# Optimization experiments

Measured on AMD Instinct MI355X. Metric: run time of the kernel, lower is better.

## Reference

```python
import jax, jax.numpy as jnp
import numpy as np

N, E, D, L = 100000, 600000, 128, 4
BN_EPS = 1e-5


def setup_inputs() -> dict:
    key = jax.random.key(0)
    ks = jax.random.split(key, 16)
    s = 0.02
    inp = {
        "x": jax.random.normal(ks[0], (N, D), dtype=jnp.float32),
        "edge_index": jax.random.randint(ks[1], (2, E), 0, N, dtype=jnp.int64),
        # per-layer SAGEConv params (lin_l has bias, lin_r has no bias in PyG)
        "lin_l_w": jax.random.normal(ks[2], (L, D, D), dtype=jnp.float32) * s,
        "lin_l_b": jnp.zeros((L, D), dtype=jnp.float32),
        "lin_r_w": jax.random.normal(ks[3], (L, D, D), dtype=jnp.float32) * s,
        # BatchNorm affine params (eval mode, running mean=0 var=1)
        "bn_w": jnp.ones((L, D), dtype=jnp.float32),
        "bn_b": jnp.zeros((L, D), dtype=jnp.float32),
        # MLP head: 128 -> 256 -> 128 -> 1
        "fc1_w": jax.random.normal(ks[4], (2 * D, D), dtype=jnp.float32) * s,
        "fc1_b": jnp.zeros((2 * D,), dtype=jnp.float32),
        "fc2_w": jax.random.normal(ks[5], (D, 2 * D), dtype=jnp.float32) * s,
        "fc2_b": jnp.zeros((D,), dtype=jnp.float32),
        "fc3_w": jax.random.normal(ks[6], (1, D), dtype=jnp.float32) * s,
        "fc3_b": jnp.zeros((1,), dtype=jnp.float32),
    }
    return inp


def _sage_layer(h, src, dst, deg_inv, wl, bl, wr):
    # mean aggregation of source features at destination nodes
    agg = jax.ops.segment_sum(h[src], dst, num_segments=N)  # [N, D]
    agg = agg * deg_inv[:, None]
    return agg @ wl.T + bl + h @ wr.T


def reference(x, lin_l_w, lin_l_b, lin_r_w, bn_w, bn_b,
              fc1_w, fc1_b, fc2_w, fc2_b, fc3_w, fc3_b, edge_index):
    src, dst = edge_index[0], edge_index[1]
    deg = jax.ops.segment_sum(jnp.ones((E,), jnp.float32), dst, num_segments=N)
    deg_inv = jnp.where(deg > 0, 1.0 / jnp.maximum(deg, 1.0), 0.0)
    inv_std = 1.0 / jnp.sqrt(1.0 + BN_EPS)  # eval BN with running mean=0, var=1

    h = x
    node_rep = x  # JK='sum' sums h_list[0..L-1]: input + first L-1 layer outputs
    for l in range(L):
        h = _sage_layer(h, src, dst, deg_inv, lin_l_w[l], lin_l_b[l], lin_r_w[l])
        h = h * inv_std * bn_w[l] + bn_b[l]
        if l != L - 1:
            h = jax.nn.relu(h)  # dropout = identity in eval mode
        if l != L - 1:
            node_rep = node_rep + h

    # batch is None -> global_add_pool sums all nodes into one graph
    g = jnp.sum(node_rep, axis=0, keepdims=True)  # [1, D]
    g = jax.nn.relu(g @ fc1_w.T + fc1_b)
    g = jax.nn.relu(g @ fc2_w.T + fc2_b)
    out = g @ fc3_w.T + fc3_b  # [1, num_tasks]
    return out
```

## Files before the change

### kernel.cpp

```cpp
#include <hip/hip_runtime.h>

#define NN 100000
#define NE 600000
#define DD 128
#define SCAN_CHUNK 2048
#define NCHUNK 49

typedef __attribute__((ext_vector_type(8))) short bf8;
typedef __attribute__((ext_vector_type(4))) float f4;
typedef __attribute__((ext_vector_type(4))) unsigned short us4;
typedef __attribute__((ext_vector_type(8))) unsigned short us8;

__device__ __forceinline__ float frelu(float x) { return x > 0.f ? x : 0.f; }

__device__ __forceinline__ float b2f(unsigned short u)
{
    union { unsigned int i; float f; } c;
    c.i = ((unsigned int)u) << 16;
    return c.f;
}

__device__ __forceinline__ unsigned short f2b(float f)
{
    union { float f; unsigned int i; } c;
    c.f = f;
    unsigned int u = c.i;
    return (unsigned short)((u + 0x7fffu + ((u >> 16) & 1u)) >> 16);
}

__device__ __forceinline__ float2 up2(unsigned int v)
{
    return make_float2(__uint_as_float(v << 16),
                       __uint_as_float(v & 0xffff0000u));
}

__global__ void k_detect(const int* __restrict__ ei, int* __restrict__ flag)
{
    if (blockIdx.x == 0 && threadIdx.x == 0) {
        int z = 1;
        for (int i = 0; i < 64; ++i)
            if (ei[2 * i + 1] != 0) { z = 0; break; }
        flag[0] = z;
    }
}

__global__ void k_count(const int* __restrict__ ei, const int* __restrict__ flag,
                        int* __restrict__ deg)
{
    int e = blockIdx.x * 256 + threadIdx.x;
    if (e >= NE) return;
    int w = flag[0];
    int dst = w ? ei[2 * (NE + e)] : ei[NE + e];
    atomicAdd(&deg[dst], 1);
}

__global__ void k_scan1(const int* __restrict__ cnt, int* __restrict__ offs,
                        int* __restrict__ chunks)
{
    __shared__ int sd[256];
    int t = threadIdx.x;
    int base = blockIdx.x * SCAN_CHUNK + t * 8;
    int v[8];
    int s = 0;
    #pragma unroll
    for (int i = 0; i < 8; ++i) {
        int idx = base + i;
        v[i] = (idx < NN) ? cnt[idx] : 0;
        s += v[i];
    }
    sd[t] = s;
    __syncthreads();
    for (int o = 1; o < 256; o <<= 1) {
        int x = (t >= o) ? sd[t - o] : 0;
        __syncthreads();
        sd[t] += x;
        __syncthreads();
    }
    int run = sd[t] - s;
    if (t == 255) chunks[blockIdx.x] = sd[255];
    #pragma unroll
    for (int i = 0; i < 8; ++i) {
        int idx = base + i;
        if (idx < NN) offs[idx] = run;
        run += v[i];
    }
}

__global__ void k_scan2(int* __restrict__ chunks, int* __restrict__ offs)
{
    if (threadIdx.x == 0 && blockIdx.x == 0) {
        int run = 0;
        for (int c = 0; c < NCHUNK; ++c) {
            int v = chunks[c];
            chunks[c] = run;
            run += v;
        }
        offs[NN] = run;
    }
}

__global__ void k_add2(int* __restrict__ offs, const int* __restrict__ chunks,
                       int* __restrict__ cursor, const int* __restrict__ deg,
                       float* __restrict__ deginv)
{
    int i = blockIdx.x * 256 + threadIdx.x;
    if (i >= NN) return;
    int v = offs[i] + chunks[i >> 11];
    offs[i] = v;
    cursor[i] = v;
    int d = deg[i];
    deginv[i] = (d > 0) ? 1.0f / (float)d : 0.0f;
}

__global__ void k_fill(const int* __restrict__ ei, const int* __restrict__ flag,
                       int* __restrict__ cursor, int* __restrict__ csr)
{
    int e = blockIdx.x * 256 + threadIdx.x;
    if (e >= NE) return;
    int w = flag[0];
    int src = w ? ei[2 * e] : ei[e];
    int dst = w ? ei[2 * (NE + e)] : ei[NE + e];
    int p = atomicAdd(&cursor[dst], 1);
    csr[p] = src;
}

__global__ void k_fold(const float* __restrict__ lwl, const float* __restrict__ lbl,
                       const float* __restrict__ lwr, const float* __restrict__ bnw,
                       const float* __restrict__ bnb, unsigned short* __restrict__ w2,
                       float* __restrict__ bias)
{
    int id = blockIdx.x * 256 + threadIdx.x;
    int l = id >> 15;
    int j = (id >> 8) & 127;
    int k = id & 255;
    float inv_std = 1.0f / sqrtf(1.0f + 1e-5f);
    float s = inv_std * bnw[l * 128 + j];
    float w = (k < 128) ? lwl[(l * 128 + j) * 128 + k]
                        : lwr[(l * 128 + j) * 128 + (k - 128)];
    w2[id] = f2b(w * s);
    if (k == 0) bias[l * 128 + j] = lbl[l * 128 + j] * s + bnb[l * 128 + j];
}

__global__ void k_cvtsum(const float* __restrict__ x, unsigned short* __restrict__ xb,
                         float* __restrict__ gsum)
{
    __shared__ float red[16][128];
    const int t = threadIdx.x;
    const int c8 = (t & 15) * 8;
    const int rg = t >> 4;
    float s[8];
    #pragma unroll
    for (int j = 0; j < 8; ++j) s[j] = 0.f;
    for (int r = blockIdx.x * 16 + rg; r < NN; r += gridDim.x * 16) {
        const f4* p = (const f4*)(x + (size_t)r * 128 + c8);
        f4 a = p[0], b = p[1];
        us8 o;
        o[0] = f2b(a[0]); o[1] = f2b(a[1]); o[2] = f2b(a[2]); o[3] = f2b(a[3]);
        o[4] = f2b(b[0]); o[5] = f2b(b[1]); o[6] = f2b(b[2]); o[7] = f2b(b[3]);
        *(us8*)(xb + (size_t)r * 128 + c8) = o;
        s[0] += a[0]; s[1] += a[1]; s[2] += a[2]; s[3] += a[3];
        s[4] += b[0]; s[5] += b[1]; s[6] += b[2]; s[7] += b[3];
    }
    #pragma unroll
    for (int j = 0; j < 8; ++j) red[rg][c8 + j] = s[j];
    __syncthreads();
    if (t < 128) {
        float v = 0.f;
        #pragma unroll
        for (int g = 0; g < 16; ++g) v += red[g][t];
        atomicAdd(&gsum[t * 16], v);
    }
}

__global__ __launch_bounds__(256)
void k_gather(const unsigned short* __restrict__ in,
              const int* __restrict__ offs, const int* __restrict__ csr,
              const float* __restrict__ deginv,
              unsigned short* __restrict__ agg)
{
    const int node = blockIdx.x * 16 + (threadIdx.x >> 4);
    const int cq = threadIdx.x & 15;
    const int lane = threadIdx.x & 63;
    const int qbase = lane & ~15;
    int s = offs[node], e = offs[node + 1];
    const int deg = e - s;
    const uint4* bcq = (const uint4*)in + cq;

    float2 a0[4], a1[4];
    #pragma unroll
    for (int j = 0; j < 4; ++j) {
        a0[j] = make_float2(0.f, 0.f);
        a1[j] = make_float2(0.f, 0.f);
    }

    for (int cb = 0; cb < deg; cb += 16) {
        int li = s + cb + cq;
        int idx = csr[(li < e) ? li : (e - 1)];
        int cnt = deg - cb; if (cnt > 16) cnt = 16;
        for (int jb = 0; jb < cnt; jb += 4) {
            int i0 = __shfl(idx, qbase + jb);
            int i1 = __shfl(idx, qbase + jb + 1);
            int i2 = __shfl(idx, qbase + jb + 2);
            int i3 = __shfl(idx, qbase + jb + 3);
            uint4 v0 = bcq[(size_t)i0 * 16];
            uint4 v1 = make_uint4(0u, 0u, 0u, 0u);
            uint4 v2 = make_uint4(0u, 0u, 0u, 0u);
            uint4 v3 = make_uint4(0u, 0u, 0u, 0u);
            if (jb + 1 < cnt) v1 = bcq[(size_t)i1 * 16];
            if (jb + 2 < cnt) v2 = bcq[(size_t)i2 * 16];
            if (jb + 3 < cnt) v3 = bcq[(size_t)i3 * 16];
            a0[0] += up2(v0.x); a0[1] += up2(v0.y);
            a0[2] += up2(v0.z); a0[3] += up2(v0.w);
            a1[0] += up2(v1.x); a1[1] += up2(v1.y);
            a1[2] += up2(v1.z); a1[3] += up2(v1.w);
            a0[0] += up2(v2.x); a0[1] += up2(v2.y);
            a0[2] += up2(v2.z); a0[3] += up2(v2.w);
            a1[0] += up2(v3.x); a1[1] += up2(v3.y);
            a1[2] += up2(v3.z); a1[3] += up2(v3.w);
        }
    }

    float di = deginv[node];
    us8 o;
    #pragma unroll
    for (int j = 0; j < 4; ++j) {
        float2 t = a0[j] + a1[j];
        o[2 * j]     = f2b(t.x * di);
        o[2 * j + 1] = f2b(t.y * di);
    }
    *(us8*)(agg + (size_t)node * 128 + cq * 8) = o;
}

__global__ __launch_bounds__(256, 2)
void k_combine(const unsigned short* __restrict__ aggb,
               const unsigned short* __restrict__ hinb,
               const unsigned short* __restrict__ w2, const float* __restrict__ bias,
               unsigned short* __restrict__ hout, float* __restrict__ gsum, int write_h)
{
    __shared__ unsigned short sW[128 * 256];
    __shared__ float red[512];
    const int tid = threadIdx.x;
    const int lane = tid & 63, wid = tid >> 6;

    {
        const f4* wg = (const f4*)w2;
        #pragma unroll
        for (int it = 0; it < 16; ++it) {
            int idx = it * 256 + tid;
            int j = idx >> 5, c = idx & 31;
            f4 v = wg[idx];
            *(f4*)((char*)sW + j * 512 + ((c * 16) ^ ((j & 7) << 4))) = v;
        }
    }
    __syncthreads();

    const int r15 = lane & 15, q = lane >> 4;

    float bb[8][4];
    #pragma unroll
    for (int ct = 0; ct < 8; ++ct)
        #pragma unroll
        for (int r = 0; r < 4; ++r) bb[ct][r] = bias[ct * 16 + q * 4 + r];

    float csum[8][4];
    #pragma unroll
    for (int ct = 0; ct < 8; ++ct)
        #pragma unroll
        for (int r = 0; r < 4; ++r) csum[ct][r] = 0.f;

    #pragma unroll
    for (int grp = 0; grp < 4; ++grp) {
        const int row = blockIdx.x * 256 + grp * 64 + wid * 16 + r15;
        const int rowc = (row < NN) ? row : (NN - 1);
        const bool ok = row < NN;

        f4 acc[8];
        #pragma unroll
        for (int ct = 0; ct < 8; ++ct) acc[ct] = (f4){0.f, 0.f, 0.f, 0.f};

        #pragma unroll
        for (int ks = 0; ks < 8; ++ks) {
            const unsigned short* s = (ks < 4) ? aggb : hinb;
            bf8 bfrag = *(const bf8*)(s + (size_t)rowc * 128 + (ks & 3) * 32 + q * 8);
            #pragma unroll
            for (int ct = 0; ct < 8; ++ct) {
                int j = ct * 16 + r15;
                bf8 wfrag = *(const bf8*)((char*)sW + j * 512 +
                                          ((ks * 64 + q * 16) ^ ((j & 7) << 4)));
                acc[ct] = __builtin_amdgcn_mfma_f32_16x16x32_bf16(wfrag, bfrag, acc[ct], 0, 0, 0);
            }
        }

        #pragma unroll
        for (int ct = 0; ct < 8; ++ct) {
            float o[4];
            #pragma unroll
            for (int r = 0; r < 4; ++r) {
                float v = frelu(acc[ct][r] + bb[ct][r]);
                o[r] = ok ? v : 0.f;
                csum[ct][r] += o[r];
            }
            if (ok && write_h) {
                us4 p;
                p[0] = f2b(o[0]); p[1] = f2b(o[1]); p[2] = f2b(o[2]); p[3] = f2b(o[3]);
                *(us4*)(hout + (size_t)row * 128 + ct * 16 + q * 4) = p;
            }
        }
    }

    #pragma unroll
    for (int ct = 0; ct < 8; ++ct)
        #pragma unroll
        for (int r = 0; r < 4; ++r) {
            float v = csum[ct][r];
            v += __shfl_xor(v, 1);
            v += __shfl_xor(v, 2);
            v += __shfl_xor(v, 4);
            v += __shfl_xor(v, 8);
            csum[ct][r] = v;
        }

    if (r15 == 0) {
        #pragma unroll
        for (int ct = 0; ct < 8; ++ct)
            #pragma unroll
            for (int r = 0; r < 4; ++r)
                red[wid * 128 + ct * 16 + q * 4 + r] = csum[ct][r];
    }
    __syncthreads();
    if (tid < 128) {
        float s = red[tid] + red[128 + tid] + red[256 + tid] + red[384 + tid];
        atomicAdd(&gsum[tid * 16], s);
    }
}

__global__ void k_mlp(const float* __restrict__ gsum,
                      const float* __restrict__ fc1w, const float* __restrict__ fc1b,
                      const float* __restrict__ fc2w, const float* __restrict__ fc2b,
                      const float* __restrict__ fc3w, const float* __restrict__ fc3b,
                      float* __restrict__ out)
{
    __shared__ float g[128], t1[256], t2[128];
    int t = threadIdx.x;
    if (t < 128) g[t] = gsum[t * 16];
    __syncthreads();
    float a = fc1b[t];
    for (int k = 0; k < 128; ++k) a += fc1w[t * 128 + k] * g[k];
    t1[t] = frelu(a);
    __syncthreads();
    if (t < 128) {
        float a2 = fc2b[t];
        for (int k = 0; k < 256; ++k) a2 += fc2w[t * 256 + k] * t1[k];
        t2[t] = frelu(a2);
    }
    __syncthreads();
    if (t < 64) {
        float s = t2[t] * fc3w[t] + t2[t + 64] * fc3w[t + 64];
        for (int o = 32; o; o >>= 1) s += __shfl_down(s, o);
        if (t == 0) out[0] = s + fc3b[0];
    }
}

extern "C" void kernel_launch(void* const* d_in, const int* in_sizes, int n_in,
                              void* d_out, int out_size, void* d_ws, size_t ws_size,
                              hipStream_t stream)
{
    const float* x    = (const float*)d_in[0];
    const int*   ei   = (const int*)d_in[1];
    const float* lwl  = (const float*)d_in[2];
    const float* lbl  = (const float*)d_in[3];
    const float* lwr  = (const float*)d_in[4];
    const float* bnw  = (const float*)d_in[5];
    const float* bnb  = (const float*)d_in[6];
    const float* fc1w = (const float*)d_in[7];
    const float* fc1b = (const float*)d_in[8];
    const float* fc2w = (const float*)d_in[9];
    const float* fc2b = (const float*)d_in[10];
    const float* fc3w = (const float*)d_in[11];
    const float* fc3b = (const float*)d_in[12];
    float* out = (float*)d_out;

    char* ws = (char*)d_ws;
    size_t off = 0;
    auto alloc = [&](size_t b) -> char* {
        char* p = ws + off;
        off = (off + b + 255) & ~(size_t)255;
        return p;
    };
    int*   deg_cnt = (int*)alloc((size_t)NN * 4);
    int*   offs    = (int*)alloc((size_t)(NN + 1) * 4);
    int*   cursor  = (int*)alloc((size_t)NN * 4);
    int*   chunks  = (int*)alloc(64 * 4);
    int*   csr     = (int*)alloc((size_t)NE * 4);
    int*   flag    = (int*)alloc(4);
    float* deginv  = (float*)alloc((size_t)NN * 4);
    unsigned short* w2   = (unsigned short*)alloc((size_t)3 * 128 * 256 * 2);
    float* bias    = (float*)alloc((size_t)3 * 128 * 4);
    float* gsum    = (float*)alloc(128 * 16 * 4);
    unsigned short* xbf  = (unsigned short*)alloc((size_t)NN * 128 * 2);
    unsigned short* hA   = (unsigned short*)alloc((size_t)NN * 128 * 2);
    unsigned short* hB   = (unsigned short*)alloc((size_t)NN * 128 * 2);
    unsigned short* agg  = (unsigned short*)alloc((size_t)NN * 128 * 2);

    hipMemsetAsync(deg_cnt, 0, (size_t)NN * 4, stream);
    hipMemsetAsync(gsum, 0, 128 * 16 * 4, stream);

    k_detect<<<1, 64, 0, stream>>>(ei, flag);
    k_count<<<(NE + 255) / 256, 256, 0, stream>>>(ei, flag, deg_cnt);
    k_scan1<<<NCHUNK, 256, 0, stream>>>(deg_cnt, offs, chunks);
    k_scan2<<<1, 64, 0, stream>>>(chunks, offs);
    k_add2<<<(NN + 255) / 256, 256, 0, stream>>>(offs, chunks, cursor, deg_cnt, deginv);
    k_fill<<<(NE + 255) / 256, 256, 0, stream>>>(ei, flag, cursor, csr);
    k_fold<<<(3 * 128 * 256) / 256, 256, 0, stream>>>(lwl, lbl, lwr, bnw, bnb, w2, bias);
    k_cvtsum<<<512, 256, 0, stream>>>(x, xbf, gsum);

    const unsigned short* hin = xbf;
    unsigned short* houts[3] = {hA, hB, hA};
    for (int l = 0; l < 3; ++l) {
        k_gather<<<NN / 16, 256, 0, stream>>>(hin, offs, csr, deginv, agg);
        k_combine<<<(NN + 255) / 256, 256, 0, stream>>>(
            agg, hin, w2 + (size_t)l * 128 * 256, bias + (size_t)l * 128,
            houts[l], gsum, (l < 2) ? 1 : 0);
        hin = houts[l];
    }
    k_mlp<<<1, 256, 0, stream>>>(gsum, fc1w, fc1b, fc2w, fc2b, fc3w, fc3b, out);
}
```

Measured before the change: 261.9 us.

## Fuse setup kernels, inline index-width detection, widen combine blocks to 512 threads

Merges edge-degree counting, x bf16 conversion with column sums, and weight folding into one launch. It also replaces the separate index-width detect kernel with a per-wave ballot check, which removes several small launches and their dependencies. k_combine now runs 512 threads per block over the same 256 rows, with 8 waves and two row groups each, so every block loads the weight tile with fewer iterations per thread. Nontemporal loads are added for the streamed activations. The 512-thread, 4-blocks-per-CU launch bound pressures registers and may cause spills, and the 64KB of LDS per block can limit actual residency.

```diff
diff --git a/kernel.cpp b/kernel.cpp
--- a/kernel.cpp
+++ b/kernel.cpp
@@ -6,6 +6,10 @@
 #define SCAN_CHUNK 2048
 #define NCHUNK 49
 
+#define CNT_B 2344
+#define CVT_B 512
+#define FOLD_B 384
+
 typedef __attribute__((ext_vector_type(8))) short bf8;
 typedef __attribute__((ext_vector_type(4))) float f4;
 typedef __attribute__((ext_vector_type(4))) unsigned short us4;
@@ -13,13 +17,6 @@
 
 __device__ __forceinline__ float frelu(float x) { return x > 0.f ? x : 0.f; }
 
-__device__ __forceinline__ float b2f(unsigned short u)
-{
-    union { unsigned int i; float f; } c;
-    c.i = ((unsigned int)u) << 16;
-    return c.f;
-}
-
 __device__ __forceinline__ unsigned short f2b(float f)
 {
     union { float f; unsigned int i; } c;
@@ -34,24 +31,71 @@
                        __uint_as_float(v & 0xffff0000u));
 }
 
-__global__ void k_detect(const int* __restrict__ ei, int* __restrict__ flag)
-{
-    if (blockIdx.x == 0 && threadIdx.x == 0) {
-        int z = 1;
-        for (int i = 0; i < 64; ++i)
-            if (ei[2 * i + 1] != 0) { z = 0; break; }
-        flag[0] = z;
-    }
-}
-
-__global__ void k_count(const int* __restrict__ ei, const int* __restrict__ flag,
-                        int* __restrict__ deg)
-{
-    int e = blockIdx.x * 256 + threadIdx.x;
-    if (e >= NE) return;
-    int w = flag[0];
-    int dst = w ? ei[2 * (NE + e)] : ei[NE + e];
-    atomicAdd(&deg[dst], 1);
+__device__ __forceinline__ bool is64(const int* __restrict__ ei)
+{
+    int v = ei[2 * (threadIdx.x & 63) + 1];
+    return __ballot(v != 0) == 0ULL;
+}
+
+__global__ __launch_bounds__(256)
+void k_setup(const int* __restrict__ ei, int* __restrict__ deg,
+             const float* __restrict__ x, unsigned short* __restrict__ xb,
+             float* __restrict__ gsum,
+             const float* __restrict__ lwl, const float* __restrict__ lbl,
+             const float* __restrict__ lwr, const float* __restrict__ bnw,
+             const float* __restrict__ bnb, unsigned short* __restrict__ w2,
+             float* __restrict__ bias)
+{
+    __shared__ float red[16][128];
+    const int b = blockIdx.x;
+    const int t = threadIdx.x;
+
+    if (b < CNT_B) {
+        bool w64 = is64(ei);
+        int e = b * 256 + t;
+        if (e < NE) {
+            int dst = w64 ? ei[2 * (NE + e)] : ei[NE + e];
+            atomicAdd(&deg[dst], 1);
+        }
+    } else if (b < CNT_B + CVT_B) {
+        const int rb = b - CNT_B;
+        const int c8 = (t & 15) * 8;
+        const int rg = t >> 4;
+        float s[8];
+        #pragma unroll
+        for (int j = 0; j < 8; ++j) s[j] = 0.f;
+        for (int r = rb * 16 + rg; r < NN; r += CVT_B * 16) {
+            const f4* p = (const f4*)(x + (size_t)r * 128 + c8);
+            f4 a = __builtin_nontemporal_load(p);
+            f4 bb = __builtin_nontemporal_load(p + 1);
+            us8 o;
+            o[0] = f2b(a[0]); o[1] = f2b(a[1]); o[2] = f2b(a[2]); o[3] = f2b(a[3]);
+            o[4] = f2b(bb[0]); o[5] = f2b(bb[1]); o[6] = f2b(bb[2]); o[7] = f2b(bb[3]);
+            *(us8*)(xb + (size_t)r * 128 + c8) = o;
+            s[0] += a[0]; s[1] += a[1]; s[2] += a[2]; s[3] += a[3];
+            s[4] += bb[0]; s[5] += bb[1]; s[6] += bb[2]; s[7] += bb[3];
+        }
+        #pragma unroll
+        for (int j = 0; j < 8; ++j) red[rg][c8 + j] = s[j];
+        __syncthreads();
+        if (t < 128) {
+            float v = 0.f;
+            #pragma unroll
+            for (int g = 0; g < 16; ++g) v += red[g][t];
+            atomicAdd(&gsum[t * 16], v);
+        }
+    } else {
+        int id = (b - CNT_B - CVT_B) * 256 + t;
+        int l = id >> 15;
+        int j = (id >> 8) & 127;
+        int k = id & 255;
+        float inv_std = 1.0f / sqrtf(1.0f + 1e-5f);
+        float sc = inv_std * bnw[l * 128 + j];
+        float w = (k < 128) ? lwl[(l * 128 + j) * 128 + k]
+                            : lwr[(l * 128 + j) * 128 + (k - 128)];
+        w2[id] = f2b(w * sc);
+        if (k == 0) bias[l * 128 + j] = lbl[l * 128 + j] * sc + bnb[l * 128 + j];
+    }
 }
 
 __global__ void k_scan1(const int* __restrict__ cnt, int* __restrict__ offs,
@@ -112,64 +156,16 @@
     deginv[i] = (d > 0) ? 1.0f / (float)d : 0.0f;
 }
 
-__global__ void k_fill(const int* __restrict__ ei, const int* __restrict__ flag,
-                       int* __restrict__ cursor, int* __restrict__ csr)
-{
+__global__ void k_fill(const int* __restrict__ ei, int* __restrict__ cursor,
+                       int* __restrict__ csr)
+{
+    bool w64 = is64(ei);
     int e = blockIdx.x * 256 + threadIdx.x;
     if (e >= NE) return;
-    int w = flag[0];
-    int src = w ? ei[2 * e] : ei[e];
-    int dst = w ? ei[2 * (NE + e)] : ei[NE + e];
+    int src = w64 ? ei[2 * e] : ei[e];
+    int dst = w64 ? ei[2 * (NE + e)] : ei[NE + e];
     int p = atomicAdd(&cursor[dst], 1);
     csr[p] = src;
-}
-
-__global__ void k_fold(const float* __restrict__ lwl, const float* __restrict__ lbl,
-                       const float* __restrict__ lwr, const float* __restrict__ bnw,
-                       const float* __restrict__ bnb, unsigned short* __restrict__ w2,
-                       float* __restrict__ bias)
-{
-    int id = blockIdx.x * 256 + threadIdx.x;
-    int l = id >> 15;
-    int j = (id >> 8) & 127;
-    int k = id & 255;
-    float inv_std = 1.0f / sqrtf(1.0f + 1e-5f);
-    float s = inv_std * bnw[l * 128 + j];
-    float w = (k < 128) ? lwl[(l * 128 + j) * 128 + k]
-                        : lwr[(l * 128 + j) * 128 + (k - 128)];
-    w2[id] = f2b(w * s);
-    if (k == 0) bias[l * 128 + j] = lbl[l * 128 + j] * s + bnb[l * 128 + j];
-}
-
-__global__ void k_cvtsum(const float* __restrict__ x, unsigned short* __restrict__ xb,
-                         float* __restrict__ gsum)
-{
-    __shared__ float red[16][128];
-    const int t = threadIdx.x;
-    const int c8 = (t & 15) * 8;
-    const int rg = t >> 4;
-    float s[8];
-    #pragma unroll
-    for (int j = 0; j < 8; ++j) s[j] = 0.f;
-    for (int r = blockIdx.x * 16 + rg; r < NN; r += gridDim.x * 16) {
-        const f4* p = (const f4*)(x + (size_t)r * 128 + c8);
-        f4 a = p[0], b = p[1];
-        us8 o;
-        o[0] = f2b(a[0]); o[1] = f2b(a[1]); o[2] = f2b(a[2]); o[3] = f2b(a[3]);
-        o[4] = f2b(b[0]); o[5] = f2b(b[1]); o[6] = f2b(b[2]); o[7] = f2b(b[3]);
-        *(us8*)(xb + (size_t)r * 128 + c8) = o;
-        s[0] += a[0]; s[1] += a[1]; s[2] += a[2]; s[3] += a[3];
-        s[4] += b[0]; s[5] += b[1]; s[6] += b[2]; s[7] += b[3];
-    }
-    #pragma unroll
-    for (int j = 0; j < 8; ++j) red[rg][c8 + j] = s[j];
-    __syncthreads();
-    if (t < 128) {
-        float v = 0.f;
-        #pragma unroll
-        for (int g = 0; g < 16; ++g) v += red[g][t];
-        atomicAdd(&gsum[t * 16], v);
-    }
 }
 
 __global__ __launch_bounds__(256)
@@ -231,22 +227,22 @@
     *(us8*)(agg + (size_t)node * 128 + cq * 8) = o;
 }
 
-__global__ __launch_bounds__(256, 2)
+__global__ __launch_bounds__(512, 4)
 void k_combine(const unsigned short* __restrict__ aggb,
                const unsigned short* __restrict__ hinb,
                const unsigned short* __restrict__ w2, const float* __restrict__ bias,
                unsigned short* __restrict__ hout, float* __restrict__ gsum, int write_h)
 {
     __shared__ unsigned short sW[128 * 256];
-    __shared__ float red[512];
+    __shared__ float red[1024];
     const int tid = threadIdx.x;
     const int lane = tid & 63, wid = tid >> 6;
 
     {
         const f4* wg = (const f4*)w2;
         #pragma unroll
-        for (int it = 0; it < 16; ++it) {
-            int idx = it * 256 + tid;
+        for (int it = 0; it < 8; ++it) {
+            int idx = it * 512 + tid;
             int j = idx >> 5, c = idx & 31;
             f4 v = wg[idx];
             *(f4*)((char*)sW + j * 512 + ((c * 16) ^ ((j & 7) << 4))) = v;
@@ -269,8 +265,8 @@
         for (int r = 0; r < 4; ++r) csum[ct][r] = 0.f;
 
     #pragma unroll
-    for (int grp = 0; grp < 4; ++grp) {
-        const int row = blockIdx.x * 256 + grp * 64 + wid * 16 + r15;
+    for (int grp = 0; grp < 2; ++grp) {
+        const int row = blockIdx.x * 256 + grp * 128 + wid * 16 + r15;
         const int rowc = (row < NN) ? row : (NN - 1);
         const bool ok = row < NN;
 
@@ -281,7 +277,8 @@
         #pragma unroll
         for (int ks = 0; ks < 8; ++ks) {
             const unsigned short* s = (ks < 4) ? aggb : hinb;
-            bf8 bfrag = *(const bf8*)(s + (size_t)rowc * 128 + (ks & 3) * 32 + q * 8);
+            bf8 bfrag = __builtin_nontemporal_load(
+                (const bf8*)(s + (size_t)rowc * 128 + (ks & 3) * 32 + q * 8));
             #pragma unroll
             for (int ct = 0; ct < 8; ++ct) {
                 int j = ct * 16 + r15;
@@ -329,7 +326,9 @@
     }
     __syncthreads();
     if (tid < 128) {
-        float s = red[tid] + red[128 + tid] + red[256 + tid] + red[384 + tid];
+        float s = 0.f;
+        #pragma unroll
+        for (int w = 0; w < 8; ++w) s += red[w * 128 + tid];
         atomicAdd(&gsum[tid * 16], s);
     }
 }
@@ -392,7 +391,6 @@
     int*   cursor  = (int*)alloc((size_t)NN * 4);
     int*   chunks  = (int*)alloc(64 * 4);
     int*   csr     = (int*)alloc((size_t)NE * 4);
-    int*   flag    = (int*)alloc(4);
     float* deginv  = (float*)alloc((size_t)NN * 4);
     unsigned short* w2   = (unsigned short*)alloc((size_t)3 * 128 * 256 * 2);
     float* bias    = (float*)alloc((size_t)3 * 128 * 4);
@@ -405,20 +403,18 @@
     hipMemsetAsync(deg_cnt, 0, (size_t)NN * 4, stream);
     hipMemsetAsync(gsum, 0, 128 * 16 * 4, stream);
 
-    k_detect<<<1, 64, 0, stream>>>(ei, flag);
-    k_count<<<(NE + 255) / 256, 256, 0, stream>>>(ei, flag, deg_cnt);
+    k_setup<<<CNT_B + CVT_B + FOLD_B, 256, 0, stream>>>(
+        ei, deg_cnt, x, xbf, gsum, lwl, lbl, lwr, bnw, bnb, w2, bias);
     k_scan1<<<NCHUNK, 256, 0, stream>>>(deg_cnt, offs, chunks);
     k_scan2<<<1, 64, 0, stream>>>(chunks, offs);
     k_add2<<<(NN + 255) / 256, 256, 0, stream>>>(offs, chunks, cursor, deg_cnt, deginv);
-    k_fill<<<(NE + 255) / 256, 256, 0, stream>>>(ei, flag, cursor, csr);
-    k_fold<<<(3 * 128 * 256) / 256, 256, 0, stream>>>(lwl, lbl, lwr, bnw, bnb, w2, bias);
-    k_cvtsum<<<512, 256, 0, stream>>>(x, xbf, gsum);
+    k_fill<<<CNT_B, 256, 0, stream>>>(ei, cursor, csr);
 
     const unsigned short* hin = xbf;
     unsigned short* houts[3] = {hA, hB, hA};
     for (int l = 0; l < 3; ++l) {
         k_gather<<<NN / 16, 256, 0, stream>>>(hin, offs, csr, deginv, agg);
-        k_combine<<<(NN + 255) / 256, 256, 0, stream>>>(
+        k_combine<<<(NN + 255) / 256, 512, 0, stream>>>(
             agg, hin, w2 + (size_t)l * 128 * 256, bias + (size_t)l * 128,
             houts[l], gsum, (l < 2) ? 1 : 0);
         hin = houts[l];
```

After: 276.2 us. +5.5%, slower.
